# Performance work log

Hardware: AMD Instinct MI355X
Metric: run time of the kernel (lower is better)

Reference implementation:

```python
import jax, jax.numpy as jnp
import numpy as np

B, S, H, NH = 4, 2048, 1024, 16
HD = H // NH

def setup_inputs() -> dict:
    key = jax.random.key(0)
    ks = jax.random.split(key, 9)
    s = 1.0 / np.sqrt(H)
    return {
        "x": jax.random.normal(ks[0], (B, S, H), dtype=jnp.float32),
        "Wq": jax.random.uniform(ks[1], (H, H), jnp.float32, -s, s),
        "bq": jax.random.uniform(ks[2], (H,), jnp.float32, -s, s),
        "Wk": jax.random.uniform(ks[3], (H, H), jnp.float32, -s, s),
        "bk": jax.random.uniform(ks[4], (H,), jnp.float32, -s, s),
        "Wv": jax.random.uniform(ks[5], (H, H), jnp.float32, -s, s),
        "bv": jax.random.uniform(ks[6], (H,), jnp.float32, -s, s),
        "Wo": jax.random.uniform(ks[7], (H, H), jnp.float32, -s, s),
        "bo": jax.random.uniform(ks[8], (H,), jnp.float32, -s, s),
    }

def reference(x, Wq, bq, Wk, bk, Wv, bv, Wo, bo):
    b, s, h = x.shape
    scale = np.sqrt(HD).astype(np.float32)
    def split_heads(t):  # [b,s,h] -> [b,nh,s,hd]
        return t.reshape(b, s, NH, HD).transpose(0, 2, 1, 3)
    Q = split_heads(x @ Wq.T + bq)
    K = split_heads(x @ Wk.T + bk)
    V = split_heads(x @ Wv.T + bv)
    scores = jnp.einsum('bnqd,bnkd->bnqk', Q, K) / scale
    weights = jax.nn.softmax(scores, axis=-1)
    attn = jnp.einsum('bnqk,bnkd->bnqd', weights, V)
    attn = attn.transpose(0, 2, 1, 3).reshape(b, s, h)
    return attn @ Wo.T + bo
```

## Files before the change

### kernel.cpp

```cpp
#include <hip/hip_runtime.h>
#include <cstdint>

#define BB 4
#define SS 2048
#define HH 1024
#define NHH 16
#define HDD 64

typedef __bf16 bf16x8 __attribute__((ext_vector_type(8)));
typedef float f32x4 __attribute__((ext_vector_type(4)));
typedef unsigned short u16x8 __attribute__((ext_vector_type(8)));

__device__ __forceinline__ unsigned short f2b(float f) {
    unsigned int u = __float_as_uint(f);
    u += 0x7fffu + ((u >> 16) & 1u);
    return (unsigned short)(u >> 16);
}

__device__ __forceinline__ void gload_lds16(const void* g, void* l) {
    __builtin_amdgcn_global_load_lds(
        (const __attribute__((address_space(1))) void*)g,
        (__attribute__((address_space(3))) void*)l, 16, 0, 0);
}

__global__ __launch_bounds__(256) void cvt_all(
    const float* __restrict__ x,
    const float* __restrict__ w0, const float* __restrict__ w1,
    const float* __restrict__ w2, const float* __restrict__ w3,
    unsigned short* __restrict__ xb, unsigned short* __restrict__ wb)
{
    const int y = blockIdx.y;
    const float* src;
    unsigned short* dst;
    if (y < 8) {
        src = x + (size_t)y * 1048576;
        dst = xb + (size_t)y * 1048576;
    } else {
        src = (y == 8) ? w0 : (y == 9) ? w1 : (y == 10) ? w2 : w3;
        dst = wb + (size_t)(y - 8) * 1048576;
    }
    long i = ((long)blockIdx.x * 256 + threadIdx.x) * 4;
    float4 v = *reinterpret_cast<const float4*>(src + i);
    ushort4 o;
    o.x = f2b(v.x); o.y = f2b(v.y); o.z = f2b(v.z); o.w = f2b(v.w);
    *reinterpret_cast<ushort4*>(dst + i) = o;
}

template<int MODE>
__global__ __launch_bounds__(256) void gemm_proj(
    const unsigned short* __restrict__ A,
    const unsigned short* __restrict__ Bm,
    const float* __restrict__ bias,
    void* __restrict__ Cout)
{
    __shared__ alignas(16) unsigned short Al[128][32];
    __shared__ alignas(16) unsigned short Bl[128][32];

    const int tid = threadIdx.x;
    const int lane = tid & 63;
    const int wid  = tid >> 6;
    const int wm = wid >> 1, wn = wid & 1;
    const int l15 = lane & 15, g = lane >> 4;
    const int row0 = blockIdx.y * 128, col0 = blockIdx.x * 128;
    const int K = HH;

    f32x4 acc[4][4];
#pragma unroll
    for (int i = 0; i < 4; i++)
#pragma unroll
        for (int j = 0; j < 4; j++) acc[i][j] = (f32x4)0.0f;

    const int off0 = tid * 16;
    const int r0s = off0 >> 6, cb0 = off0 & 63;
    const int off1 = off0 + 4096;
    const int r1s = off1 >> 6, cb1 = off1 & 63;

    for (int k0 = 0; k0 < K; k0 += 32) {
        const char* gA = (const char*)(A + (size_t)row0 * K + k0);
        const char* gB = (const char*)(Bm + (size_t)col0 * K + k0);
        char* lA = (char*)&Al[0][0] + wid * 1024;
        char* lB = (char*)&Bl[0][0] + wid * 1024;
        gload_lds16(gA + (size_t)r0s * (K * 2) + cb0, lA);
        gload_lds16(gA + (size_t)r1s * (K * 2) + cb1, lA + 4096);
        gload_lds16(gB + (size_t)r0s * (K * 2) + cb0, lB);
        gload_lds16(gB + (size_t)r1s * (K * 2) + cb1, lB + 4096);
        __syncthreads();

        bf16x8 af[4], bf[4];
#pragma unroll
        for (int i = 0; i < 4; i++)
            af[i] = *reinterpret_cast<const bf16x8*>(&Al[wm * 64 + i * 16 + l15][g * 8]);
#pragma unroll
        for (int j = 0; j < 4; j++)
            bf[j] = *reinterpret_cast<const bf16x8*>(&Bl[wn * 64 + j * 16 + l15][g * 8]);
        __builtin_amdgcn_s_setprio(1);
#pragma unroll
        for (int i = 0; i < 4; i++)
#pragma unroll
            for (int j = 0; j < 4; j++)
                acc[i][j] = __builtin_amdgcn_mfma_f32_16x16x32_bf16(af[i], bf[j], acc[i][j], 0, 0, 0);
        __builtin_amdgcn_s_setprio(0);
        __syncthreads();
    }

#pragma unroll
    for (int i = 0; i < 4; i++) {
#pragma unroll
        for (int j = 0; j < 4; j++) {
#pragma unroll
            for (int r = 0; r < 4; r++) {
                int row = row0 + wm * 64 + i * 16 + g * 4 + r;
                int col = col0 + wn * 64 + j * 16 + l15;
                float v = acc[i][j][r] + bias[col];
                if (MODE == 0) {
                    reinterpret_cast<unsigned short*>(Cout)[(size_t)row * HH + col] = f2b(v);
                } else if (MODE == 1) {
                    int b = row >> 11;
                    int s = row & (SS - 1);
                    int s6 = s & 63;
                    int sp6 = (s6 & 0x23) | ((s6 & 0x0C) << 1) | ((s6 & 0x10) >> 2);
                    int head = col >> 6;
                    int d = col & (HDD - 1);
                    size_t idx = (((size_t)b * NHH + head) * HDD + d) * SS + (s & ~63) + sp6;
                    reinterpret_cast<unsigned short*>(Cout)[idx] = f2b(v);
                } else {
                    reinterpret_cast<float*>(Cout)[(size_t)row * HH + col] = v;
                }
            }
        }
    }
}

__global__ __launch_bounds__(256, 4) void attn_kernel(
    const unsigned short* __restrict__ Q,
    const unsigned short* __restrict__ K,
    const unsigned short* __restrict__ Vt,
    unsigned short* __restrict__ Oa)
{
    __shared__ alignas(16) unsigned short Kf[2][8][64][8];
    __shared__ alignas(16) unsigned short Vf[2][8][64][8];

    const int tid = threadIdx.x;
    const int lane = tid & 63;
    const int wid  = tid >> 6;
    const int l15 = lane & 15, g = lane >> 4;

    const int wg = blockIdx.x;
    const int L = (wg & 7) * 128 + (wg >> 3);
    const int qt = L & 15;
    const int bh = L >> 4;
    const int b  = bh >> 4;
    const int h  = bh & 15;
    const int q0 = qt * 128;
    const int qA = q0 + wid * 32;

    const float qs = 0.125f * 1.44269504088896f;
    const unsigned short* qpA = Q + (size_t)(b * SS + qA + l15) * HH + h * HDD + g * 8;
    const unsigned short* qpB = qpA + (size_t)16 * HH;
    u16x8 ra0 = *reinterpret_cast<const u16x8*>(qpA);
    u16x8 ra1 = *reinterpret_cast<const u16x8*>(qpA + 32);
    u16x8 rb0 = *reinterpret_cast<const u16x8*>(qpB);
    u16x8 rb1 = *reinterpret_cast<const u16x8*>(qpB + 32);
#pragma unroll
    for (int j = 0; j < 8; j++) {
        ra0[j] = f2b(__uint_as_float((unsigned)ra0[j] << 16) * qs);
        ra1[j] = f2b(__uint_as_float((unsigned)ra1[j] << 16) * qs);
        rb0[j] = f2b(__uint_as_float((unsigned)rb0[j] << 16) * qs);
        rb1[j] = f2b(__uint_as_float((unsigned)rb1[j] << 16) * qs);
    }
    const bf16x8 qa0 = __builtin_bit_cast(bf16x8, ra0);
    const bf16x8 qa1 = __builtin_bit_cast(bf16x8, ra1);
    const bf16x8 qb0 = __builtin_bit_cast(bf16x8, rb0);
    const bf16x8 qb1 = __builtin_bit_cast(bf16x8, rb1);

    u16x8 ou;
#pragma unroll
    for (int j = 0; j < 8; j++) ou[j] = 0x3F80;
    const bf16x8 ones8 = __builtin_bit_cast(bf16x8, ou);
    const f32x4 zero4 = (f32x4)0.0f;

    f32x4 acc_a[4], acc_b[4];
#pragma unroll
    for (int dn = 0; dn < 4; dn++) { acc_a[dn] = zero4; acc_b[dn] = zero4; }
    f32x4 lacc_a = zero4, lacc_b = zero4;

    const int krow = wid * 16 + l15;
    const unsigned short* gKs = K  + (size_t)(b * SS + krow) * HH + h * HDD + (lane >> 4) * 8;
    const unsigned short* gVs = Vt + (((size_t)b * NHH + h) * HDD + krow) * SS + (lane >> 4) * 8;
    char* kdst = (char*)&Kf[0][2 * wid][0][0];
    char* vdst = (char*)&Vf[0][2 * wid][0][0];

    auto STAGE = [&](int buf, int kt) {
        const unsigned short* pk = gKs + (size_t)(kt * 64) * HH;
        const unsigned short* pv = gVs + kt * 64;
        gload_lds16(pk,      kdst + buf * 8192);
        gload_lds16(pk + 32, kdst + buf * 8192 + 1024);
        gload_lds16(pv,      vdst + buf * 8192);
        gload_lds16(pv + 32, vdst + buf * 8192 + 1024);
    };

    auto pack2 = [](float lo, float hi) -> unsigned {
        return (__float_as_uint(hi) & 0xFFFF0000u) | (__float_as_uint(lo) >> 16);
    };

    const int NT = SS / 64;
    STAGE(0, 0);
    int cur = 0;

    for (int kt = 0; kt < NT; kt++) {
        if (kt + 1 < NT) {
            STAGE(cur ^ 1, kt + 1);
            asm volatile("s_waitcnt vmcnt(4)" ::: "memory");
        } else {
            asm volatile("s_waitcnt vmcnt(0)" ::: "memory");
        }
        __builtin_amdgcn_s_barrier();

        f32x4 sa[4], sb[4];
        __builtin_amdgcn_s_setprio(1);
#pragma unroll
        for (int n = 0; n < 4; n++) {
            bf16x8 kf0 = *reinterpret_cast<const bf16x8*>(&Kf[cur][n * 2 + 0][lane][0]);
            bf16x8 kf1 = *reinterpret_cast<const bf16x8*>(&Kf[cur][n * 2 + 1][lane][0]);
            sa[n] = __builtin_amdgcn_mfma_f32_16x16x32_bf16(kf0, qa0, zero4, 0, 0, 0);
            sa[n] = __builtin_amdgcn_mfma_f32_16x16x32_bf16(kf1, qa1, sa[n], 0, 0, 0);
            sb[n] = __builtin_amdgcn_mfma_f32_16x16x32_bf16(kf0, qb0, zero4, 0, 0, 0);
            sb[n] = __builtin_amdgcn_mfma_f32_16x16x32_bf16(kf1, qb1, sb[n], 0, 0, 0);
        }
        __builtin_amdgcn_s_setprio(0);

        float pA[4][4], pB[4][4];
#pragma unroll
        for (int n = 0; n < 4; n++)
#pragma unroll
            for (int r = 0; r < 4; r++) {
                pA[n][r] = __builtin_amdgcn_exp2f(sa[n][r]);
                pB[n][r] = __builtin_amdgcn_exp2f(sb[n][r]);
            }
        uint4 wa0, wa1, wb0, wb1;
        wa0.x = pack2(pA[0][0], pA[0][1]); wa0.y = pack2(pA[0][2], pA[0][3]);
        wa0.z = pack2(pA[1][0], pA[1][1]); wa0.w = pack2(pA[1][2], pA[1][3]);
        wa1.x = pack2(pA[2][0], pA[2][1]); wa1.y = pack2(pA[2][2], pA[2][3]);
        wa1.z = pack2(pA[3][0], pA[3][1]); wa1.w = pack2(pA[3][2], pA[3][3]);
        wb0.x = pack2(pB[0][0], pB[0][1]); wb0.y = pack2(pB[0][2], pB[0][3]);
        wb0.z = pack2(pB[1][0], pB[1][1]); wb0.w = pack2(pB[1][2], pB[1][3]);
        wb1.x = pack2(pB[2][0], pB[2][1]); wb1.y = pack2(pB[2][2], pB[2][3]);
        wb1.z = pack2(pB[3][0], pB[3][1]); wb1.w = pack2(pB[3][2], pB[3][3]);
        const bf16x8 pa0 = __builtin_bit_cast(bf16x8, wa0);
        const bf16x8 pa1 = __builtin_bit_cast(bf16x8, wa1);
        const bf16x8 pb0 = __builtin_bit_cast(bf16x8, wb0);
        const bf16x8 pb1 = __builtin_bit_cast(bf16x8, wb1);

        __builtin_amdgcn_s_setprio(1);
#pragma unroll
        for (int ks = 0; ks < 2; ks++) {
            bf16x8 pAf = ks ? pa1 : pa0;
            bf16x8 pBf = ks ? pb1 : pb0;
#pragma unroll
            for (int dn = 0; dn < 4; dn++) {
                bf16x8 vf = *reinterpret_cast<const bf16x8*>(&Vf[cur][dn * 2 + ks][lane][0]);
                acc_a[dn] = __builtin_amdgcn_mfma_f32_16x16x32_bf16(vf, pAf, acc_a[dn], 0, 0, 0);
                acc_b[dn] = __builtin_amdgcn_mfma_f32_16x16x32_bf16(vf, pBf, acc_b[dn], 0, 0, 0);
            }
        }
        lacc_a = __builtin_amdgcn_mfma_f32_16x16x32_bf16(ones8, pa0, lacc_a, 0, 0, 0);
        lacc_a = __builtin_amdgcn_mfma_f32_16x16x32_bf16(ones8, pa1, lacc_a, 0, 0, 0);
        lacc_b = __builtin_amdgcn_mfma_f32_16x16x32_bf16(ones8, pb0, lacc_b, 0, 0, 0);
        lacc_b = __builtin_amdgcn_mfma_f32_16x16x32_bf16(ones8, pb1, lacc_b, 0, 0, 0);
        __builtin_amdgcn_s_setprio(0);

        __builtin_amdgcn_s_barrier();
        cur ^= 1;
    }

    float inv_a = 1.0f / lacc_a[0];
    float inv_b = 1.0f / lacc_b[0];
    unsigned short* oA = Oa + (size_t)(b * SS + qA + l15) * HH + h * HDD;
    unsigned short* oB = oA + (size_t)16 * HH;
#pragma unroll
    for (int dn = 0; dn < 4; dn++) {
        ushort4 wa, wb;
        wa.x = f2b(acc_a[dn][0] * inv_a); wa.y = f2b(acc_a[dn][1] * inv_a);
        wa.z = f2b(acc_a[dn][2] * inv_a); wa.w = f2b(acc_a[dn][3] * inv_a);
        wb.x = f2b(acc_b[dn][0] * inv_b); wb.y = f2b(acc_b[dn][1] * inv_b);
        wb.z = f2b(acc_b[dn][2] * inv_b); wb.w = f2b(acc_b[dn][3] * inv_b);
        *reinterpret_cast<ushort4*>(oA + dn * 16 + g * 4) = wa;
        *reinterpret_cast<ushort4*>(oB + dn * 16 + g * 4) = wb;
    }
}

extern "C" void kernel_launch(void* const* d_in, const int* in_sizes, int n_in,
                              void* d_out, int out_size, void* d_ws, size_t ws_size,
                              hipStream_t stream) {
    const float* x  = (const float*)d_in[0];
    const float* Wq = (const float*)d_in[1];
    const float* bq = (const float*)d_in[2];
    const float* Wk = (const float*)d_in[3];
    const float* bk = (const float*)d_in[4];
    const float* Wv = (const float*)d_in[5];
    const float* bv = (const float*)d_in[6];
    const float* Wo = (const float*)d_in[7];
    const float* bo = (const float*)d_in[8];
    float* out = (float*)d_out;

    const int M = BB * SS;

    unsigned char* ws = (unsigned char*)d_ws;
    unsigned short* xb  = (unsigned short*)(ws);
    unsigned short* Wqb = (unsigned short*)(ws + 16777216);
    unsigned short* Wkb = (unsigned short*)(ws + 16777216 + 2097152);
    unsigned short* Wvb = (unsigned short*)(ws + 16777216 + 2 * 2097152);
    unsigned short* Wob = (unsigned short*)(ws + 16777216 + 3 * 2097152);
    unsigned short* Qb  = (unsigned short*)(ws + 16777216 + 4 * 2097152);
    unsigned short* Kb  = (unsigned short*)(ws + 2 * 16777216 + 4 * 2097152);
    unsigned short* Vtb = (unsigned short*)(ws + 3 * 16777216 + 4 * 2097152);
    unsigned short* Ab  = (unsigned short*)(ws + 4 * 16777216 + 4 * 2097152);

    cvt_all<<<dim3(1024, 12), 256, 0, stream>>>(x, Wq, Wk, Wv, Wo, xb, Wqb);

    dim3 ggrid(HH / 128, M / 128);
    gemm_proj<0><<<ggrid, 256, 0, stream>>>(xb, Wqb, bq, Qb);
    gemm_proj<0><<<ggrid, 256, 0, stream>>>(xb, Wkb, bk, Kb);
    gemm_proj<1><<<ggrid, 256, 0, stream>>>(xb, Wvb, bv, Vtb);

    attn_kernel<<<1024, 256, 0, stream>>>(Qb, Kb, Vtb, Ab);

    gemm_proj<2><<<ggrid, 256, 0, stream>>>(Ab, Wob, bo, out);
}
```

Measured before the change: 210.6 us.

## Give each attention wave 64 query rows with two waves per block

The attention kernel now runs 2 waves per block instead of 4, and each wave handles 64 query rows (four 16-row chunks) instead of 32. Each K/V fragment read from LDS is therefore reused across four query chunks, which halves LDS reads per MFMA. Each wave also issues twice as many K/V staging loads. The exp2 and pack work is interleaved directly after each score MFMA. The cost is many more accumulator registers per wave (16 f32x4 accumulators), a lower launch-bounds occupancy hint, and fewer waves per block to hide latency.

```diff
diff --git a/kernel.cpp b/kernel.cpp
--- a/kernel.cpp
+++ b/kernel.cpp
@@ -131,7 +131,7 @@
     }
 }
 
-__global__ __launch_bounds__(256, 4) void attn_kernel(
+__global__ __launch_bounds__(128, 2) void attn_kernel(
     const unsigned short* __restrict__ Q,
     const unsigned short* __restrict__ K,
     const unsigned short* __restrict__ Vt,
@@ -152,26 +152,23 @@
     const int b  = bh >> 4;
     const int h  = bh & 15;
     const int q0 = qt * 128;
-    const int qA = q0 + wid * 32;
+    const int qW = q0 + wid * 64;
 
     const float qs = 0.125f * 1.44269504088896f;
-    const unsigned short* qpA = Q + (size_t)(b * SS + qA + l15) * HH + h * HDD + g * 8;
-    const unsigned short* qpB = qpA + (size_t)16 * HH;
-    u16x8 ra0 = *reinterpret_cast<const u16x8*>(qpA);
-    u16x8 ra1 = *reinterpret_cast<const u16x8*>(qpA + 32);
-    u16x8 rb0 = *reinterpret_cast<const u16x8*>(qpB);
-    u16x8 rb1 = *reinterpret_cast<const u16x8*>(qpB + 32);
-#pragma unroll
-    for (int j = 0; j < 8; j++) {
-        ra0[j] = f2b(__uint_as_float((unsigned)ra0[j] << 16) * qs);
-        ra1[j] = f2b(__uint_as_float((unsigned)ra1[j] << 16) * qs);
-        rb0[j] = f2b(__uint_as_float((unsigned)rb0[j] << 16) * qs);
-        rb1[j] = f2b(__uint_as_float((unsigned)rb1[j] << 16) * qs);
-    }
-    const bf16x8 qa0 = __builtin_bit_cast(bf16x8, ra0);
-    const bf16x8 qa1 = __builtin_bit_cast(bf16x8, ra1);
-    const bf16x8 qb0 = __builtin_bit_cast(bf16x8, rb0);
-    const bf16x8 qb1 = __builtin_bit_cast(bf16x8, rb1);
+    bf16x8 qf0[4], qf1[4];
+#pragma unroll
+    for (int c = 0; c < 4; c++) {
+        const unsigned short* qp = Q + (size_t)(b * SS + qW + c * 16 + l15) * HH + h * HDD + g * 8;
+        u16x8 r0 = *reinterpret_cast<const u16x8*>(qp);
+        u16x8 r1 = *reinterpret_cast<const u16x8*>(qp + 32);
+#pragma unroll
+        for (int j = 0; j < 8; j++) {
+            r0[j] = f2b(__uint_as_float((unsigned)r0[j] << 16) * qs);
+            r1[j] = f2b(__uint_as_float((unsigned)r1[j] << 16) * qs);
+        }
+        qf0[c] = __builtin_bit_cast(bf16x8, r0);
+        qf1[c] = __builtin_bit_cast(bf16x8, r1);
+    }
 
     u16x8 ou;
 #pragma unroll
@@ -179,24 +176,37 @@
     const bf16x8 ones8 = __builtin_bit_cast(bf16x8, ou);
     const f32x4 zero4 = (f32x4)0.0f;
 
-    f32x4 acc_a[4], acc_b[4];
-#pragma unroll
-    for (int dn = 0; dn < 4; dn++) { acc_a[dn] = zero4; acc_b[dn] = zero4; }
-    f32x4 lacc_a = zero4, lacc_b = zero4;
-
-    const int krow = wid * 16 + l15;
-    const unsigned short* gKs = K  + (size_t)(b * SS + krow) * HH + h * HDD + (lane >> 4) * 8;
-    const unsigned short* gVs = Vt + (((size_t)b * NHH + h) * HDD + krow) * SS + (lane >> 4) * 8;
-    char* kdst = (char*)&Kf[0][2 * wid][0][0];
-    char* vdst = (char*)&Vf[0][2 * wid][0][0];
+    f32x4 acc[4][4];
+#pragma unroll
+    for (int c = 0; c < 4; c++)
+#pragma unroll
+        for (int dn = 0; dn < 4; dn++) acc[c][dn] = zero4;
+    f32x4 lacc[4];
+#pragma unroll
+    for (int c = 0; c < 4; c++) lacc[c] = zero4;
+
+    const int row0k = (2 * wid + 0) * 16 + l15;
+    const int row1k = (2 * wid + 1) * 16 + l15;
+    const unsigned short* gK0 = K + (size_t)(b * SS + row0k) * HH + h * HDD + g * 8;
+    const unsigned short* gK1 = K + (size_t)(b * SS + row1k) * HH + h * HDD + g * 8;
+    const unsigned short* gV0 = Vt + (((size_t)b * NHH + h) * HDD + row0k) * SS + g * 8;
+    const unsigned short* gV1 = Vt + (((size_t)b * NHH + h) * HDD + row1k) * SS + g * 8;
+    char* kd0 = (char*)&Kf[0][(2 * wid + 0) * 2][0][0];
+    char* kd1 = (char*)&Kf[0][(2 * wid + 1) * 2][0][0];
+    char* vd0 = (char*)&Vf[0][(2 * wid + 0) * 2][0][0];
+    char* vd1 = (char*)&Vf[0][(2 * wid + 1) * 2][0][0];
 
     auto STAGE = [&](int buf, int kt) {
-        const unsigned short* pk = gKs + (size_t)(kt * 64) * HH;
-        const unsigned short* pv = gVs + kt * 64;
-        gload_lds16(pk,      kdst + buf * 8192);
-        gload_lds16(pk + 32, kdst + buf * 8192 + 1024);
-        gload_lds16(pv,      vdst + buf * 8192);
-        gload_lds16(pv + 32, vdst + buf * 8192 + 1024);
+        const size_t ko = (size_t)(kt * 64) * HH;
+        const int vo = kt * 64;
+        gload_lds16(gK0 + ko,      kd0 + buf * 8192);
+        gload_lds16(gK0 + ko + 32, kd0 + buf * 8192 + 1024);
+        gload_lds16(gK1 + ko,      kd1 + buf * 8192);
+        gload_lds16(gK1 + ko + 32, kd1 + buf * 8192 + 1024);
+        gload_lds16(gV0 + vo,      vd0 + buf * 8192);
+        gload_lds16(gV0 + vo + 32, vd0 + buf * 8192 + 1024);
+        gload_lds16(gV1 + vo,      vd1 + buf * 8192);
+        gload_lds16(gV1 + vo + 32, vd1 + buf * 8192 + 1024);
     };
 
     auto pack2 = [](float lo, float hi) -> unsigned {
@@ -210,82 +220,76 @@
     for (int kt = 0; kt < NT; kt++) {
         if (kt + 1 < NT) {
             STAGE(cur ^ 1, kt + 1);
-            asm volatile("s_waitcnt vmcnt(4)" ::: "memory");
+            asm volatile("s_waitcnt vmcnt(8)" ::: "memory");
         } else {
             asm volatile("s_waitcnt vmcnt(0)" ::: "memory");
         }
         __builtin_amdgcn_s_barrier();
 
-        f32x4 sa[4], sb[4];
+        unsigned pw[4][8];
         __builtin_amdgcn_s_setprio(1);
 #pragma unroll
         for (int n = 0; n < 4; n++) {
             bf16x8 kf0 = *reinterpret_cast<const bf16x8*>(&Kf[cur][n * 2 + 0][lane][0]);
             bf16x8 kf1 = *reinterpret_cast<const bf16x8*>(&Kf[cur][n * 2 + 1][lane][0]);
-            sa[n] = __builtin_amdgcn_mfma_f32_16x16x32_bf16(kf0, qa0, zero4, 0, 0, 0);
-            sa[n] = __builtin_amdgcn_mfma_f32_16x16x32_bf16(kf1, qa1, sa[n], 0, 0, 0);
-            sb[n] = __builtin_amdgcn_mfma_f32_16x16x32_bf16(kf0, qb0, zero4, 0, 0, 0);
-            sb[n] = __builtin_amdgcn_mfma_f32_16x16x32_bf16(kf1, qb1, sb[n], 0, 0, 0);
+#pragma unroll
+            for (int c = 0; c < 4; c++) {
+                f32x4 s = __builtin_amdgcn_mfma_f32_16x16x32_bf16(kf0, qf0[c], zero4, 0, 0, 0);
+                s = __builtin_amdgcn_mfma_f32_16x16x32_bf16(kf1, qf1[c], s, 0, 0, 0);
+                float p0 = __builtin_amdgcn_exp2f(s[0]);
+                float p1 = __builtin_amdgcn_exp2f(s[1]);
+                float p2 = __builtin_amdgcn_exp2f(s[2]);
+                float p3 = __builtin_amdgcn_exp2f(s[3]);
+                pw[c][n * 2]     = pack2(p0, p1);
+                pw[c][n * 2 + 1] = pack2(p2, p3);
+            }
         }
         __builtin_amdgcn_s_setprio(0);
 
-        float pA[4][4], pB[4][4];
-#pragma unroll
-        for (int n = 0; n < 4; n++)
-#pragma unroll
-            for (int r = 0; r < 4; r++) {
-                pA[n][r] = __builtin_amdgcn_exp2f(sa[n][r]);
-                pB[n][r] = __builtin_amdgcn_exp2f(sb[n][r]);
-            }
-        uint4 wa0, wa1, wb0, wb1;
-        wa0.x = pack2(pA[0][0], pA[0][1]); wa0.y = pack2(pA[0][2], pA[0][3]);
-        wa0.z = pack2(pA[1][0], pA[1][1]); wa0.w = pack2(pA[1][2], pA[1][3]);
-        wa1.x = pack2(pA[2][0], pA[2][1]); wa1.y = pack2(pA[2][2], pA[2][3]);
-        wa1.z = pack2(pA[3][0], pA[3][1]); wa1.w = pack2(pA[3][2], pA[3][3]);
-        wb0.x = pack2(pB[0][0], pB[0][1]); wb0.y = pack2(pB[0][2], pB[0][3]);
-        wb0.z = pack2(pB[1][0], pB[1][1]); wb0.w = pack2(pB[1][2], pB[1][3]);
-        wb1.x = pack2(pB[2][0], pB[2][1]); wb1.y = pack2(pB[2][2], pB[2][3]);
-        wb1.z = pack2(pB[3][0], pB[3][1]); wb1.w = pack2(pB[3][2], pB[3][3]);
-        const bf16x8 pa0 = __builtin_bit_cast(bf16x8, wa0);
-        const bf16x8 pa1 = __builtin_bit_cast(bf16x8, wa1);
-        const bf16x8 pb0 = __builtin_bit_cast(bf16x8, wb0);
-        const bf16x8 pb1 = __builtin_bit_cast(bf16x8, wb1);
+        bf16x8 pk0[4], pk1[4];
+#pragma unroll
+        for (int c = 0; c < 4; c++) {
+            uint4 w0 = { pw[c][0], pw[c][1], pw[c][2], pw[c][3] };
+            uint4 w1 = { pw[c][4], pw[c][5], pw[c][6], pw[c][7] };
+            pk0[c] = __builtin_bit_cast(bf16x8, w0);
+            pk1[c] = __builtin_bit_cast(bf16x8, w1);
+        }
 
         __builtin_amdgcn_s_setprio(1);
 #pragma unroll
         for (int ks = 0; ks < 2; ks++) {
-            bf16x8 pAf = ks ? pa1 : pa0;
-            bf16x8 pBf = ks ? pb1 : pb0;
 #pragma unroll
             for (int dn = 0; dn < 4; dn++) {
                 bf16x8 vf = *reinterpret_cast<const bf16x8*>(&Vf[cur][dn * 2 + ks][lane][0]);
-                acc_a[dn] = __builtin_amdgcn_mfma_f32_16x16x32_bf16(vf, pAf, acc_a[dn], 0, 0, 0);
-                acc_b[dn] = __builtin_amdgcn_mfma_f32_16x16x32_bf16(vf, pBf, acc_b[dn], 0, 0, 0);
+#pragma unroll
+                for (int c = 0; c < 4; c++) {
+                    bf16x8 pf = ks ? pk1[c] : pk0[c];
+                    acc[c][dn] = __builtin_amdgcn_mfma_f32_16x16x32_bf16(vf, pf, acc[c][dn], 0, 0, 0);
+                }
             }
         }
-        lacc_a = __builtin_amdgcn_mfma_f32_16x16x32_bf16(ones8, pa0, lacc_a, 0, 0, 0);
-        lacc_a = __builtin_amdgcn_mfma_f32_16x16x32_bf16(ones8, pa1, lacc_a, 0, 0, 0);
-        lacc_b = __builtin_amdgcn_mfma_f32_16x16x32_bf16(ones8, pb0, lacc_b, 0, 0, 0);
-        lacc_b = __builtin_amdgcn_mfma_f32_16x16x32_bf16(ones8, pb1, lacc_b, 0, 0, 0);
+#pragma unroll
+        for (int c = 0; c < 4; c++) {
+            lacc[c] = __builtin_amdgcn_mfma_f32_16x16x32_bf16(ones8, pk0[c], lacc[c], 0, 0, 0);
+            lacc[c] = __builtin_amdgcn_mfma_f32_16x16x32_bf16(ones8, pk1[c], lacc[c], 0, 0, 0);
+        }
         __builtin_amdgcn_s_setprio(0);
 
         __builtin_amdgcn_s_barrier();
         cur ^= 1;
     }
 
-    float inv_a = 1.0f / lacc_a[0];
-    float inv_b = 1.0f / lacc_b[0];
-    unsigned short* oA = Oa + (size_t)(b * SS + qA + l15) * HH + h * HDD;
-    unsigned short* oB = oA + (size_t)16 * HH;
-#pragma unroll
-    for (int dn = 0; dn < 4; dn++) {
-        ushort4 wa, wb;
-        wa.x = f2b(acc_a[dn][0] * inv_a); wa.y = f2b(acc_a[dn][1] * inv_a);
-        wa.z = f2b(acc_a[dn][2] * inv_a); wa.w = f2b(acc_a[dn][3] * inv_a);
-        wb.x = f2b(acc_b[dn][0] * inv_b); wb.y = f2b(acc_b[dn][1] * inv_b);
-        wb.z = f2b(acc_b[dn][2] * inv_b); wb.w = f2b(acc_b[dn][3] * inv_b);
-        *reinterpret_cast<ushort4*>(oA + dn * 16 + g * 4) = wa;
-        *reinterpret_cast<ushort4*>(oB + dn * 16 + g * 4) = wb;
+#pragma unroll
+    for (int c = 0; c < 4; c++) {
+        float inv = 1.0f / lacc[c][0];
+        unsigned short* oP = Oa + (size_t)(b * SS + qW + c * 16 + l15) * HH + h * HDD;
+#pragma unroll
+        for (int dn = 0; dn < 4; dn++) {
+            ushort4 w;
+            w.x = f2b(acc[c][dn][0] * inv); w.y = f2b(acc[c][dn][1] * inv);
+            w.z = f2b(acc[c][dn][2] * inv); w.w = f2b(acc[c][dn][3] * inv);
+            *reinterpret_cast<ushort4*>(oP + dn * 16 + g * 4) = w;
+        }
     }
 }
 
@@ -323,7 +327,7 @@
     gemm_proj<0><<<ggrid, 256, 0, stream>>>(xb, Wkb, bk, Kb);
     gemm_proj<1><<<ggrid, 256, 0, stream>>>(xb, Wvb, bv, Vtb);
 
-    attn_kernel<<<1024, 256, 0, stream>>>(Qb, Kb, Vtb, Ab);
+    attn_kernel<<<1024, 128, 0, stream>>>(Qb, Kb, Vtb, Ab);
 
     gemm_proj<2><<<ggrid, 256, 0, stream>>>(Ab, Wob, bo, out);
 }
```

Result: no change. 211.1 us (+0.2%).

## Double-buffer LDS tiles in projection GEMM with async prefetch

Applied to the files above, without the earlier changes.

Adds a second LDS buffer for the A and B tiles in the projection GEMM. The next K-slice is issued with global_load_lds before the current slice's MFMAs run, and a partial vmcnt wait lets the load overlap with compute. The intent is to hide global-to-LDS latency that the single-buffer loop exposed at each iteration. It doubles LDS use per block and depends on hand-placed waitcnt and barrier instructions being correct.

```diff
diff --git a/kernel.cpp b/kernel.cpp
--- a/kernel.cpp
+++ b/kernel.cpp
@@ -53,8 +53,8 @@
     const float* __restrict__ bias,
     void* __restrict__ Cout)
 {
-    __shared__ alignas(16) unsigned short Al[128][32];
-    __shared__ alignas(16) unsigned short Bl[128][32];
+    __shared__ alignas(16) unsigned short Al[2][128][32];
+    __shared__ alignas(16) unsigned short Bl[2][128][32];
 
     const int tid = threadIdx.x;
     const int lane = tid & 63;
@@ -75,24 +75,41 @@
     const int off1 = off0 + 4096;
     const int r1s = off1 >> 6, cb1 = off1 & 63;
 
-    for (int k0 = 0; k0 < K; k0 += 32) {
-        const char* gA = (const char*)(A + (size_t)row0 * K + k0);
-        const char* gB = (const char*)(Bm + (size_t)col0 * K + k0);
-        char* lA = (char*)&Al[0][0] + wid * 1024;
-        char* lB = (char*)&Bl[0][0] + wid * 1024;
-        gload_lds16(gA + (size_t)r0s * (K * 2) + cb0, lA);
-        gload_lds16(gA + (size_t)r1s * (K * 2) + cb1, lA + 4096);
-        gload_lds16(gB + (size_t)r0s * (K * 2) + cb0, lB);
-        gload_lds16(gB + (size_t)r1s * (K * 2) + cb1, lB + 4096);
-        __syncthreads();
+    const char* gAb = (const char*)(A + (size_t)row0 * K);
+    const char* gBb = (const char*)(Bm + (size_t)col0 * K);
+    const int aoff0 = r0s * (K * 2) + cb0;
+    const int aoff1 = r1s * (K * 2) + cb1;
+
+    auto STAGE = [&](int buf, int t) {
+        const char* a = gAb + t * 64;
+        const char* bsrc = gBb + t * 64;
+        char* lA = (char*)&Al[buf][0][0] + wid * 1024;
+        char* lB = (char*)&Bl[buf][0][0] + wid * 1024;
+        gload_lds16(a + aoff0, lA);
+        gload_lds16(a + aoff1, lA + 4096);
+        gload_lds16(bsrc + aoff0, lB);
+        gload_lds16(bsrc + aoff1, lB + 4096);
+    };
+
+    STAGE(0, 0);
+    int cur = 0;
+
+    for (int k = 0; k < 32; k++) {
+        if (k < 31) {
+            STAGE(cur ^ 1, k + 1);
+            asm volatile("s_waitcnt vmcnt(4)" ::: "memory");
+        } else {
+            asm volatile("s_waitcnt vmcnt(0)" ::: "memory");
+        }
+        __builtin_amdgcn_s_barrier();
 
         bf16x8 af[4], bf[4];
 #pragma unroll
         for (int i = 0; i < 4; i++)
-            af[i] = *reinterpret_cast<const bf16x8*>(&Al[wm * 64 + i * 16 + l15][g * 8]);
+            af[i] = *reinterpret_cast<const bf16x8*>(&Al[cur][wm * 64 + i * 16 + l15][g * 8]);
 #pragma unroll
         for (int j = 0; j < 4; j++)
-            bf[j] = *reinterpret_cast<const bf16x8*>(&Bl[wn * 64 + j * 16 + l15][g * 8]);
+            bf[j] = *reinterpret_cast<const bf16x8*>(&Bl[cur][wn * 64 + j * 16 + l15][g * 8]);
         __builtin_amdgcn_s_setprio(1);
 #pragma unroll
         for (int i = 0; i < 4; i++)
@@ -100,7 +117,9 @@
             for (int j = 0; j < 4; j++)
                 acc[i][j] = __builtin_amdgcn_mfma_f32_16x16x32_bf16(af[i], bf[j], acc[i][j], 0, 0, 0);
         __builtin_amdgcn_s_setprio(0);
-        __syncthreads();
+
+        __builtin_amdgcn_s_barrier();
+        cur ^= 1;
     }
 
 #pragma unroll
```

Result: slower. 220.3 us (+4.6%).
